# Kernel optimization log

Measured on AMD Instinct MI355X. Metric: run time of the kernel, lower is better.

Reference implementation:

```python
import jax, jax.numpy as jnp
import numpy as np

DIM = 768
NUM_HEADS = 8
HEAD_DIM = DIM // NUM_HEADS


def setup_inputs() -> dict:
    key = jax.random.key(0)
    ks = jax.random.split(key, 5)
    B, N, C = 16, 4096, DIM
    x = jax.random.normal(ks[0], (B, N, C), dtype=jnp.float32)
    # nn.Linear(dim, dim*3): weight [3C, C], bias [3C]
    w_qkv = jax.random.normal(ks[1], (3 * C, C), dtype=jnp.float32) * (C ** -0.5)
    b_qkv = jax.random.normal(ks[2], (3 * C,), dtype=jnp.float32) * 0.02
    w_proj = jax.random.normal(ks[3], (C, C), dtype=jnp.float32) * (C ** -0.5)
    b_proj = jax.random.normal(ks[4], (C,), dtype=jnp.float32) * 0.02
    return {"x": x, "w_qkv": w_qkv, "b_qkv": b_qkv, "w_proj": w_proj, "b_proj": b_proj}


def reference(x, w_qkv, b_qkv, w_proj, b_proj):
    B, N, C = x.shape
    H, D = NUM_HEADS, C // NUM_HEADS
    # qkv projection: [B,N,3C] -> [3,B,H,N,D]
    qkv = x @ w_qkv.T + b_qkv
    qkv = qkv.reshape(B, N, 3, H, D).transpose(2, 0, 3, 1, 4)
    q, k, v = qkv[0], qkv[1], qkv[2]
    # dynamic_scale=True: scale by N^-0.5
    q = q * (N ** -0.5)
    # channel attention: contract over tokens N -> [B,H,D,D]
    attn = jnp.einsum("bhnd,bhne->bhde", q, k)
    attn = jax.nn.softmax(attn, axis=-1)
    # (attn @ v^T)^T -> [B,H,N,D]
    out = jnp.einsum("bhde,bhne->bhnd", attn, v)
    out = out.transpose(0, 2, 1, 3).reshape(B, N, C)
    return out @ w_proj.T + b_proj
```

## Files before the change

kernel.cpp:

```cpp
#include <hip/hip_runtime.h>
#include <hip/hip_bf16.h>
#include <stdint.h>

typedef __bf16 bf16;
typedef __bf16 bf16x8 __attribute__((ext_vector_type(8)));
typedef __bf16 bf16x4 __attribute__((ext_vector_type(4)));
typedef float f32x4 __attribute__((ext_vector_type(4)));

__device__ __forceinline__ void gl_lds16(const bf16* g, bf16* l) {
  __builtin_amdgcn_global_load_lds(
      (const __attribute__((address_space(1))) void*)g,
      (__attribute__((address_space(3))) void*)l, 16, 0, 0);
}

__global__ void cvt_f32_bf16(const float* __restrict__ in, bf16* __restrict__ out, int n4) {
  int i = blockIdx.x * blockDim.x + threadIdx.x;
  if (i < n4) {
    float4 v = ((const float4*)in)[i];
    bf16x4 o;
    o[0] = (bf16)v.x; o[1] = (bf16)v.y; o[2] = (bf16)v.z; o[3] = (bf16)v.w;
    ((bf16x4*)out)[i] = o;
  }
}

template<int EPI>
__global__ __launch_bounds__(256) void gemm_bt(
    const bf16* __restrict__ A, const bf16* __restrict__ B,
    const float* __restrict__ bias, void* __restrict__ Cout,
    int M, int N, int K, int nbn)
{
  __shared__ __align__(16) bf16 sA[128 * 32];
  __shared__ __align__(16) bf16 sB[128 * 32];
  int bm = blockIdx.x / nbn, bn = blockIdx.x % nbn;
  int m0 = bm * 128, n0 = bn * 128;
  int t = threadIdx.x;
  int wave = t >> 6, lane = t & 63;
  int wm = wave >> 1, wn = wave & 1;
  int l16 = lane & 15, quad = lane >> 4;

  f32x4 acc[4][4] = {};

  int rA = (wave * 2) * 16 + (lane >> 2);
  int kk = (lane & 3) * 8;
  const bf16* gA = A + (long)(m0 + rA) * K + kk;
  const bf16* gB = B + (long)(n0 + rA) * K + kk;

  for (int k0 = 0; k0 < K; k0 += 32) {
    gl_lds16(gA + k0,            &sA[(wave * 2) * 512]);
    gl_lds16(gA + 16 * K + k0,   &sA[(wave * 2 + 1) * 512]);
    gl_lds16(gB + k0,            &sB[(wave * 2) * 512]);
    gl_lds16(gB + 16 * K + k0,   &sB[(wave * 2 + 1) * 512]);
    __syncthreads();
    bf16x8 af[4], bfr[4];
#pragma unroll
    for (int mi = 0; mi < 4; mi++)
      af[mi] = *(const bf16x8*)&sA[(wm * 64 + mi * 16 + l16) * 32 + quad * 8];
#pragma unroll
    for (int ni = 0; ni < 4; ni++)
      bfr[ni] = *(const bf16x8*)&sB[(wn * 64 + ni * 16 + l16) * 32 + quad * 8];
#pragma unroll
    for (int mi = 0; mi < 4; mi++)
#pragma unroll
      for (int ni = 0; ni < 4; ni++)
        acc[mi][ni] = __builtin_amdgcn_mfma_f32_16x16x32_bf16(af[mi], bfr[ni], acc[mi][ni], 0, 0, 0);
    __syncthreads();
  }

#pragma unroll
  for (int mi = 0; mi < 4; mi++) {
    int row = m0 + wm * 64 + mi * 16 + quad * 4;
#pragma unroll
    for (int ni = 0; ni < 4; ni++) {
      int col = n0 + wn * 64 + ni * 16 + l16;
      float bv = bias[col];
#pragma unroll
      for (int r = 0; r < 4; r++) {
        float v = acc[mi][ni][r] + bv;
        if (EPI == 0) {
          if (col < 768) v *= 0.015625f;
          ((bf16*)Cout)[(long)(row + r) * N + col] = (bf16)v;
        } else {
          ((float*)Cout)[(long)(row + r) * N + col] = v;
        }
      }
    }
  }
}

__global__ __launch_bounds__(256) void attn_qk(const bf16* __restrict__ qkv, float* __restrict__ part)
{
  __shared__ __align__(16) bf16 sQ[96 * 72];
  __shared__ __align__(16) bf16 sK[96 * 72];
  int bh = blockIdx.x >> 1, kb = blockIdx.x & 1;
  int b = bh >> 3, h = bh & 7;
  int t = threadIdx.x;
  int wave = t >> 6, lane = t & 63;
  int wm = wave >> 1, wn = wave & 1;
  int l16 = lane & 15, quad = lane >> 4;
  f32x4 acc[3][3] = {};
  const bf16* Qb = qkv + (long)b * 4096 * 2304 + h * 96;
  const bf16* Kb = Qb + 768;

  for (int it = 0; it < 32; it++) {
    int tok0 = kb * 2048 + it * 64;
    __syncthreads();
#pragma unroll
    for (int i = 0; i < 3; i++) {
      int id = i * 256 + t;
      int tl = id / 12, cc = id % 12;
      uint4 q4 = *(const uint4*)(Qb + (long)(tok0 + tl) * 2304 + cc * 8);
      uint4 k4 = *(const uint4*)(Kb + (long)(tok0 + tl) * 2304 + cc * 8);
      const bf16* qe = (const bf16*)&q4;
      const bf16* ke = (const bf16*)&k4;
#pragma unroll
      for (int j = 0; j < 8; j++) {
        sQ[(cc * 8 + j) * 72 + tl] = qe[j];
        sK[(cc * 8 + j) * 72 + tl] = ke[j];
      }
    }
    __syncthreads();
#pragma unroll
    for (int ks = 0; ks < 2; ks++) {
      bf16x8 af[3], bfr[3];
#pragma unroll
      for (int mi = 0; mi < 3; mi++)
        af[mi] = *(const bf16x8*)&sQ[(wm * 48 + mi * 16 + l16) * 72 + ks * 32 + quad * 8];
#pragma unroll
      for (int ni = 0; ni < 3; ni++)
        bfr[ni] = *(const bf16x8*)&sK[(wn * 48 + ni * 16 + l16) * 72 + ks * 32 + quad * 8];
#pragma unroll
      for (int mi = 0; mi < 3; mi++)
#pragma unroll
        for (int ni = 0; ni < 3; ni++)
          acc[mi][ni] = __builtin_amdgcn_mfma_f32_16x16x32_bf16(af[mi], bfr[ni], acc[mi][ni], 0, 0, 0);
    }
  }
  float* pout = part + (long)(bh * 2 + kb) * 9216;
#pragma unroll
  for (int mi = 0; mi < 3; mi++)
#pragma unroll
    for (int ni = 0; ni < 3; ni++) {
      int row = wm * 48 + mi * 16 + quad * 4;
      int col = wn * 48 + ni * 16 + l16;
#pragma unroll
      for (int r = 0; r < 4; r++)
        pout[(row + r) * 96 + col] = acc[mi][ni][r];
    }
}

__global__ __launch_bounds__(256) void softmax_attn(const float* __restrict__ part, bf16* __restrict__ attn)
{
  __shared__ float s[96 * 97];
  int bh = blockIdx.x;
  int t = threadIdx.x;
  const float* p0 = part + (long)bh * 2 * 9216;
  const float* p1 = p0 + 9216;
  for (int e = t; e < 9216; e += 256) {
    int r = e / 96, c = e % 96;
    s[r * 97 + c] = p0[e] + p1[e];
  }
  __syncthreads();
  if (t < 96) {
    float m = -1e30f;
    for (int i = 0; i < 96; i++) m = fmaxf(m, s[t * 97 + i]);
    float sum = 0.f;
    for (int i = 0; i < 96; i++) {
      float ev = __expf(s[t * 97 + i] - m);
      s[t * 97 + i] = ev;
      sum += ev;
    }
    float inv = 1.f / sum;
    bf16* ao = attn + (long)bh * 9216 + t * 96;
    for (int i = 0; i < 96; i++) ao[i] = (bf16)(s[t * 97 + i] * inv);
  }
}

__global__ __launch_bounds__(256) void attn_v(
    const bf16* __restrict__ qkv, const bf16* __restrict__ attn, bf16* __restrict__ out2)
{
  __shared__ __align__(16) bf16 sV[128 * 96];
  __shared__ __align__(16) bf16 sAt[96 * 96];
  int bh = blockIdx.x >> 5, tb = blockIdx.x & 31;
  int b = bh >> 3, h = bh & 7;
  int tok0 = tb * 128;
  int t = threadIdx.x;
  int wave = t >> 6, lane = t & 63;
  int wm = wave >> 1, wn = wave & 1;
  int l16 = lane & 15, quad = lane >> 4;
  f32x4 acc[4][3] = {};
  const bf16* Vb = qkv + (long)b * 4096 * 2304 + 1536 + h * 96;

#pragma unroll
  for (int j = 0; j < 6; j++) {
    int c = wave * 6 + j;
    int g = c * 64 + lane;
    int tok = g / 12, cc = g % 12;
    gl_lds16(Vb + (long)(tok0 + tok) * 2304 + cc * 8, &sV[c * 512]);
  }
  for (int c = wave; c < 18; c += 4) {
    int g = c * 64 + lane;
    int d = g / 12, cc = g % 12;
    gl_lds16(attn + (long)bh * 9216 + d * 96 + cc * 8, &sAt[c * 512]);
  }
  __syncthreads();
#pragma unroll
  for (int ks = 0; ks < 3; ks++) {
    bf16x8 af[4], bfr[3];
#pragma unroll
    for (int mi = 0; mi < 4; mi++)
      af[mi] = *(const bf16x8*)&sV[(wm * 64 + mi * 16 + l16) * 96 + ks * 32 + quad * 8];
#pragma unroll
    for (int ni = 0; ni < 3; ni++)
      bfr[ni] = *(const bf16x8*)&sAt[(wn * 48 + ni * 16 + l16) * 96 + ks * 32 + quad * 8];
#pragma unroll
    for (int mi = 0; mi < 4; mi++)
#pragma unroll
      for (int ni = 0; ni < 3; ni++)
        acc[mi][ni] = __builtin_amdgcn_mfma_f32_16x16x32_bf16(af[mi], bfr[ni], acc[mi][ni], 0, 0, 0);
  }
  bf16* ob = out2 + (long)(b * 4096 + tok0) * 768 + h * 96;
#pragma unroll
  for (int mi = 0; mi < 4; mi++)
#pragma unroll
    for (int ni = 0; ni < 3; ni++) {
      int row = wm * 64 + mi * 16 + quad * 4;
      int col = wn * 48 + ni * 16 + l16;
#pragma unroll
      for (int r = 0; r < 4; r++)
        ob[(long)(row + r) * 768 + col] = (bf16)acc[mi][ni][r];
    }
}

extern "C" void kernel_launch(void* const* d_in, const int* in_sizes, int n_in,
                              void* d_out, int out_size, void* d_ws, size_t ws_size,
                              hipStream_t stream) {
  const float* x      = (const float*)d_in[0];
  const float* w_qkv  = (const float*)d_in[1];
  const float* b_qkv  = (const float*)d_in[2];
  const float* w_proj = (const float*)d_in[3];
  const float* b_proj = (const float*)d_in[4];

  char* ws = (char*)d_ws;
  bf16*  Xb     = (bf16*)ws;
  bf16*  Wqkvb  = (bf16*)(ws + 100663296);
  bf16*  Wprojb = (bf16*)(ws + 104202240);
  bf16*  qkvb   = (bf16*)(ws + 105381888);
  float* part   = (float*)(ws + 407371776);
  bf16*  attnb  = (bf16*)(ws + 416808960);
  bf16*  out2   = (bf16*)ws;

  cvt_f32_bf16<<<(12582912 + 255) / 256, 256, 0, stream>>>(x, Xb, 12582912);
  cvt_f32_bf16<<<(442368 + 255) / 256, 256, 0, stream>>>(w_qkv, Wqkvb, 442368);
  cvt_f32_bf16<<<(147456 + 255) / 256, 256, 0, stream>>>(w_proj, Wprojb, 147456);

  gemm_bt<0><<<512 * 18, 256, 0, stream>>>(Xb, Wqkvb, b_qkv, qkvb, 65536, 2304, 768, 18);
  attn_qk<<<256, 256, 0, stream>>>(qkvb, part);
  softmax_attn<<<128, 256, 0, stream>>>(part, attnb);
  attn_v<<<4096, 256, 0, stream>>>(qkvb, attnb, out2);
  gemm_bt<1><<<512 * 6, 256, 0, stream>>>(out2, Wprojb, b_proj, d_out, 65536, 768, 768, 6);
}
```

Before: 939.7 us.

## Store Q/K transposed from QKV GEMM and split QK reduction wider

The QKV GEMM epilogue now writes Q and K in a token-contiguous transposed layout and V into its own compact buffer, so attn_qk can stream tiles with direct global-to-LDS loads instead of scalar transposing stores into shared memory. The QK^T reduction is split into 8 token slices per head (1024 blocks instead of 256) to improve occupancy, and the softmax kernel sums 8 partials. The GEMM also remaps block indices to interleave tiles across groups. The transposed epilogue writes 4-element strided chunks, which may hurt store coalescing in the large GEMM.

```diff
diff --git a/kernel.cpp b/kernel.cpp
--- a/kernel.cpp
+++ b/kernel.cpp
@@ -26,12 +26,15 @@
 template<int EPI>
 __global__ __launch_bounds__(256) void gemm_bt(
     const bf16* __restrict__ A, const bf16* __restrict__ B,
-    const float* __restrict__ bias, void* __restrict__ Cout,
-    int M, int N, int K, int nbn)
+    const float* __restrict__ bias, void* __restrict__ C0, void* __restrict__ C1,
+    void* __restrict__ C2, int M, int N, int K, int nbn)
 {
   __shared__ __align__(16) bf16 sA[128 * 32];
   __shared__ __align__(16) bf16 sB[128 * 32];
-  int bm = blockIdx.x / nbn, bn = blockIdx.x % nbn;
+  int tiles = gridDim.x;
+  int bid = blockIdx.x;
+  int tile = ((bid & 7) * (tiles >> 3)) + (bid >> 3);
+  int bm = tile / nbn, bn = tile % nbn;
   int m0 = bm * 128, n0 = bn * 128;
   int t = threadIdx.x;
   int wave = t >> 6, lane = t & 63;
@@ -46,10 +49,10 @@
   const bf16* gB = B + (long)(n0 + rA) * K + kk;
 
   for (int k0 = 0; k0 < K; k0 += 32) {
-    gl_lds16(gA + k0,            &sA[(wave * 2) * 512]);
-    gl_lds16(gA + 16 * K + k0,   &sA[(wave * 2 + 1) * 512]);
-    gl_lds16(gB + k0,            &sB[(wave * 2) * 512]);
-    gl_lds16(gB + 16 * K + k0,   &sB[(wave * 2 + 1) * 512]);
+    gl_lds16(gA + k0,          &sA[(wave * 2) * 512]);
+    gl_lds16(gA + 16 * K + k0, &sA[(wave * 2 + 1) * 512]);
+    gl_lds16(gB + k0,          &sB[(wave * 2) * 512]);
+    gl_lds16(gB + 16 * K + k0, &sB[(wave * 2 + 1) * 512]);
     __syncthreads();
     bf16x8 af[4], bfr[4];
 #pragma unroll
@@ -66,76 +69,100 @@
     __syncthreads();
   }
 
-#pragma unroll
-  for (int mi = 0; mi < 4; mi++) {
-    int row = m0 + wm * 64 + mi * 16 + quad * 4;
-#pragma unroll
-    for (int ni = 0; ni < 4; ni++) {
-      int col = n0 + wn * 64 + ni * 16 + l16;
-      float bv = bias[col];
-#pragma unroll
-      for (int r = 0; r < 4; r++) {
-        float v = acc[mi][ni][r] + bv;
-        if (EPI == 0) {
-          if (col < 768) v *= 0.015625f;
-          ((bf16*)Cout)[(long)(row + r) * N + col] = (bf16)v;
-        } else {
-          ((float*)Cout)[(long)(row + r) * N + col] = v;
-        }
+  if (EPI == 1) {
+#pragma unroll
+    for (int mi = 0; mi < 4; mi++) {
+      int row = m0 + wm * 64 + mi * 16 + quad * 4;
+#pragma unroll
+      for (int ni = 0; ni < 4; ni++) {
+        int col = n0 + wn * 64 + ni * 16 + l16;
+        float bv = bias[col];
+#pragma unroll
+        for (int r = 0; r < 4; r++)
+          ((float*)C0)[(long)(row + r) * N + col] = acc[mi][ni][r] + bv;
       }
     }
-  }
-}
-
-__global__ __launch_bounds__(256) void attn_qk(const bf16* __restrict__ qkv, float* __restrict__ part)
-{
-  __shared__ __align__(16) bf16 sQ[96 * 72];
-  __shared__ __align__(16) bf16 sK[96 * 72];
-  int bh = blockIdx.x >> 1, kb = blockIdx.x & 1;
+  } else if (n0 < 1536) {
+    bf16* T = (n0 < 768) ? (bf16*)C0 : (bf16*)C1;
+    int coff = (n0 < 768) ? 0 : 768;
+    float scale = (n0 < 768) ? 0.015625f : 1.0f;
+    int b = m0 >> 12;
+    int tokB = m0 & 4095;
+#pragma unroll
+    for (int mi = 0; mi < 4; mi++) {
+      int tokN = tokB + wm * 64 + mi * 16 + quad * 4;
+#pragma unroll
+      for (int ni = 0; ni < 4; ni++) {
+        int col = n0 + wn * 64 + ni * 16 + l16;
+        float bv = bias[col];
+        bf16x4 o;
+#pragma unroll
+        for (int r = 0; r < 4; r++) o[r] = (bf16)((acc[mi][ni][r] + bv) * scale);
+        *(bf16x4*)&T[((long)(b * 768 + (col - coff))) * 4096 + tokN] = o;
+      }
+    }
+  } else {
+    bf16* V = (bf16*)C2;
+#pragma unroll
+    for (int mi = 0; mi < 4; mi++) {
+      int row = m0 + wm * 64 + mi * 16 + quad * 4;
+#pragma unroll
+      for (int ni = 0; ni < 4; ni++) {
+        int col = n0 + wn * 64 + ni * 16 + l16;
+        float bv = bias[col];
+#pragma unroll
+        for (int r = 0; r < 4; r++)
+          V[(long)(row + r) * 768 + (col - 1536)] = (bf16)(acc[mi][ni][r] + bv);
+      }
+    }
+  }
+}
+
+__global__ __launch_bounds__(256) void attn_qk(
+    const bf16* __restrict__ qT, const bf16* __restrict__ kT, float* __restrict__ part)
+{
+  __shared__ __align__(16) bf16 sQ[96 * 32];
+  __shared__ __align__(16) bf16 sK[96 * 32];
+  int bid = blockIdx.x;
+  int bh = bid >> 3, s = bid & 7;
   int b = bh >> 3, h = bh & 7;
   int t = threadIdx.x;
   int wave = t >> 6, lane = t & 63;
   int wm = wave >> 1, wn = wave & 1;
   int l16 = lane & 15, quad = lane >> 4;
   f32x4 acc[3][3] = {};
-  const bf16* Qb = qkv + (long)b * 4096 * 2304 + h * 96;
-  const bf16* Kb = Qb + 768;
-
-  for (int it = 0; it < 32; it++) {
-    int tok0 = kb * 2048 + it * 64;
-    __syncthreads();
-#pragma unroll
-    for (int i = 0; i < 3; i++) {
-      int id = i * 256 + t;
-      int tl = id / 12, cc = id % 12;
-      uint4 q4 = *(const uint4*)(Qb + (long)(tok0 + tl) * 2304 + cc * 8);
-      uint4 k4 = *(const uint4*)(Kb + (long)(tok0 + tl) * 2304 + cc * 8);
-      const bf16* qe = (const bf16*)&q4;
-      const bf16* ke = (const bf16*)&k4;
-#pragma unroll
-      for (int j = 0; j < 8; j++) {
-        sQ[(cc * 8 + j) * 72 + tl] = qe[j];
-        sK[(cc * 8 + j) * 72 + tl] = ke[j];
-      }
-    }
-    __syncthreads();
-#pragma unroll
-    for (int ks = 0; ks < 2; ks++) {
-      bf16x8 af[3], bfr[3];
-#pragma unroll
-      for (int mi = 0; mi < 3; mi++)
-        af[mi] = *(const bf16x8*)&sQ[(wm * 48 + mi * 16 + l16) * 72 + ks * 32 + quad * 8];
+  const bf16* Qb = qT + ((long)(b * 768 + h * 96)) * 4096 + s * 512;
+  const bf16* Kb = kT + ((long)(b * 768 + h * 96)) * 4096 + s * 512;
+
+  int rowc = lane >> 2;
+  int ko = (lane & 3) * 8;
+
+  for (int it = 0; it < 16; it++) {
+#pragma unroll
+    for (int j = 0; j < 3; j++) {
+      int c2 = wave * 3 + j;
+      int c = (c2 < 6) ? c2 : c2 - 6;
+      int row = c * 16 + rowc;
+      const bf16* src = ((c2 < 6) ? Qb : Kb) + (long)row * 4096 + it * 32 + ko;
+      bf16* dst = ((c2 < 6) ? sQ : sK) + c * 512;
+      gl_lds16(src, dst);
+    }
+    __syncthreads();
+    bf16x8 af[3], bfr[3];
+#pragma unroll
+    for (int mi = 0; mi < 3; mi++)
+      af[mi] = *(const bf16x8*)&sQ[(wm * 48 + mi * 16 + l16) * 32 + quad * 8];
+#pragma unroll
+    for (int ni = 0; ni < 3; ni++)
+      bfr[ni] = *(const bf16x8*)&sK[(wn * 48 + ni * 16 + l16) * 32 + quad * 8];
+#pragma unroll
+    for (int mi = 0; mi < 3; mi++)
 #pragma unroll
       for (int ni = 0; ni < 3; ni++)
-        bfr[ni] = *(const bf16x8*)&sK[(wn * 48 + ni * 16 + l16) * 72 + ks * 32 + quad * 8];
-#pragma unroll
-      for (int mi = 0; mi < 3; mi++)
-#pragma unroll
-        for (int ni = 0; ni < 3; ni++)
-          acc[mi][ni] = __builtin_amdgcn_mfma_f32_16x16x32_bf16(af[mi], bfr[ni], acc[mi][ni], 0, 0, 0);
-    }
-  }
-  float* pout = part + (long)(bh * 2 + kb) * 9216;
+        acc[mi][ni] = __builtin_amdgcn_mfma_f32_16x16x32_bf16(af[mi], bfr[ni], acc[mi][ni], 0, 0, 0);
+    __syncthreads();
+  }
+  float* pout = part + (long)bid * 9216;
 #pragma unroll
   for (int mi = 0; mi < 3; mi++)
 #pragma unroll
@@ -153,11 +180,13 @@
   __shared__ float s[96 * 97];
   int bh = blockIdx.x;
   int t = threadIdx.x;
-  const float* p0 = part + (long)bh * 2 * 9216;
-  const float* p1 = p0 + 9216;
+  const float* p0 = part + (long)bh * 8 * 9216;
   for (int e = t; e < 9216; e += 256) {
+    float v = 0.f;
+#pragma unroll
+    for (int k = 0; k < 8; k++) v += p0[k * 9216 + e];
     int r = e / 96, c = e % 96;
-    s[r * 97 + c] = p0[e] + p1[e];
+    s[r * 97 + c] = v;
   }
   __syncthreads();
   if (t < 96) {
@@ -176,7 +205,7 @@
 }
 
 __global__ __launch_bounds__(256) void attn_v(
-    const bf16* __restrict__ qkv, const bf16* __restrict__ attn, bf16* __restrict__ out2)
+    const bf16* __restrict__ V, const bf16* __restrict__ attn, bf16* __restrict__ out2)
 {
   __shared__ __align__(16) bf16 sV[128 * 96];
   __shared__ __align__(16) bf16 sAt[96 * 96];
@@ -188,14 +217,14 @@
   int wm = wave >> 1, wn = wave & 1;
   int l16 = lane & 15, quad = lane >> 4;
   f32x4 acc[4][3] = {};
-  const bf16* Vb = qkv + (long)b * 4096 * 2304 + 1536 + h * 96;
+  const bf16* Vb = V + (long)b * 4096 * 768 + h * 96;
 
 #pragma unroll
   for (int j = 0; j < 6; j++) {
     int c = wave * 6 + j;
     int g = c * 64 + lane;
     int tok = g / 12, cc = g % 12;
-    gl_lds16(Vb + (long)(tok0 + tok) * 2304 + cc * 8, &sV[c * 512]);
+    gl_lds16(Vb + (long)(tok0 + tok) * 768 + cc * 8, &sV[c * 512]);
   }
   for (int c = wave; c < 18; c += 4) {
     int g = c * 64 + lane;
@@ -242,20 +271,22 @@
 
   char* ws = (char*)d_ws;
   bf16*  Xb     = (bf16*)ws;
+  float* part   = (float*)ws;
+  bf16*  out2   = (bf16*)ws;
   bf16*  Wqkvb  = (bf16*)(ws + 100663296);
   bf16*  Wprojb = (bf16*)(ws + 104202240);
-  bf16*  qkvb   = (bf16*)(ws + 105381888);
-  float* part   = (float*)(ws + 407371776);
-  bf16*  attnb  = (bf16*)(ws + 416808960);
-  bf16*  out2   = (bf16*)ws;
+  bf16*  qT     = (bf16*)(ws + 105381888);
+  bf16*  kT     = (bf16*)(ws + 206045184);
+  bf16*  Vbuf   = (bf16*)(ws + 306708480);
+  bf16*  attnb  = (bf16*)(ws + 407371776);
 
   cvt_f32_bf16<<<(12582912 + 255) / 256, 256, 0, stream>>>(x, Xb, 12582912);
   cvt_f32_bf16<<<(442368 + 255) / 256, 256, 0, stream>>>(w_qkv, Wqkvb, 442368);
   cvt_f32_bf16<<<(147456 + 255) / 256, 256, 0, stream>>>(w_proj, Wprojb, 147456);
 
-  gemm_bt<0><<<512 * 18, 256, 0, stream>>>(Xb, Wqkvb, b_qkv, qkvb, 65536, 2304, 768, 18);
-  attn_qk<<<256, 256, 0, stream>>>(qkvb, part);
+  gemm_bt<0><<<512 * 18, 256, 0, stream>>>(Xb, Wqkvb, b_qkv, qT, kT, Vbuf, 65536, 2304, 768, 18);
+  attn_qk<<<1024, 256, 0, stream>>>(qT, kT, part);
   softmax_attn<<<128, 256, 0, stream>>>(part, attnb);
-  attn_v<<<4096, 256, 0, stream>>>(qkvb, attnb, out2);
-  gemm_bt<1><<<512 * 6, 256, 0, stream>>>(out2, Wprojb, b_proj, d_out, 65536, 768, 768, 6);
-}
+  attn_v<<<4096, 256, 0, stream>>>(Vbuf, attnb, out2);
+  gemm_bt<1><<<512 * 6, 256, 0, stream>>>(out2, Wprojb, b_proj, d_out, nullptr, nullptr, 65536, 768, 768, 6);
+}
```

Result: slower. 981.5 us (+4.5%).
